# Optimization experiments

Measured on AMD Instinct MI355X. Metric: run time of the kernel, lower is better.

The kernel has to match this reference:

```python
import jax, jax.numpy as jnp
import numpy as np

BETA = 0.25  # commitment_cost


def setup_inputs() -> dict:
    key = jax.random.key(0)
    k1, k2 = jax.random.split(key)
    N, K, D = 32768, 8192, 512
    z = jax.random.normal(k1, (N, D), dtype=jnp.float32)
    # mimic nn.init.uniform_(codebook, -1/K, 1/K)
    codebook = jax.random.uniform(k2, (K, D), dtype=jnp.float32,
                                  minval=-1.0 / K, maxval=1.0 / K)
    return {"z": z, "codebook": codebook}


def reference(z, codebook):
    # squared L2 distances: ||z||^2 + ||c||^2 - 2 z c^T   -> [N, K]
    d = (jnp.sum(z * z, axis=1, keepdims=True)
         + jnp.sum(codebook * codebook, axis=1)
         - 2.0 * (z @ codebook.T))
    indices = jnp.argmin(d, axis=1)            # [N] int
    z_q = codebook[indices]                    # [N, D] gather (grad flows to codebook)
    # commit_loss = beta * mse(z.detach(), z_q)
    commit_loss = BETA * jnp.mean((jax.lax.stop_gradient(z) - z_q) ** 2)
    # straight-through estimator
    z_st = z + jax.lax.stop_gradient(z_q - z)
    return z_st, indices, commit_loss
```

## Files before the change

### kernel.cpp

```cpp
#include <hip/hip_runtime.h>
#include <cfloat>
#include <cstdint>
#include <cstddef>

#define N_ROWS 32768
#define K_CODES 8192
#define DIM 512
#define BETA 0.25

typedef unsigned short u16;
typedef _Float16 half8 __attribute__((ext_vector_type(8)));
typedef float f32x4 __attribute__((ext_vector_type(4)));

#define BM 256
#define BN 256
#define BKH 64
#define NKT (DIM / BKH)
#define OVCAP 512
#define DELTA_A 0.4f

#define GLOAD_LDS16(g, l)                                          \
  __builtin_amdgcn_global_load_lds(                                \
      (const __attribute__((address_space(1))) void*)(g),          \
      (__attribute__((address_space(3))) void*)(l), 16, 0, 0)

__device__ inline u16 f2h(float x) {
  union { _Float16 h; u16 u; } c;
  c.h = (_Float16)x;
  return c.u;
}

__global__ __launch_bounds__(256)
void vq_cvt(const float* __restrict__ src, u16* __restrict__ dst, float scale,
            int n8, int* ovcnt_reset) {
  if (ovcnt_reset != nullptr && blockIdx.x == 0 && threadIdx.x == 0) *ovcnt_reset = 0;
  int i = blockIdx.x * 256 + threadIdx.x;
  if (i >= n8) return;
  float4 a = ((const float4*)src)[(size_t)i * 2];
  float4 b = ((const float4*)src)[(size_t)i * 2 + 1];
  uint4 o;
  o.x = (unsigned)f2h(a.x * scale) | ((unsigned)f2h(a.y * scale) << 16);
  o.y = (unsigned)f2h(a.z * scale) | ((unsigned)f2h(a.w * scale) << 16);
  o.z = (unsigned)f2h(b.x * scale) | ((unsigned)f2h(b.y * scale) << 16);
  o.w = (unsigned)f2h(b.z * scale) | ((unsigned)f2h(b.w * scale) << 16);
  ((uint4*)dst)[i] = o;
}

__global__ __launch_bounds__(256)
void vq_s1(const float* __restrict__ z, float* __restrict__ s1out) {
  int row = blockIdx.x * 256 + threadIdx.x;
  const float* p = z + (size_t)row * DIM;
  float lf[4];
#pragma unroll
  for (int L = 0; L < 4; ++L) {
    const float* q = p + L * 128;
    float r[8];
#pragma unroll
    for (int j = 0; j < 8; ++j) r[j] = __fmul_rn(q[j], q[j]);
    for (int i = 8; i < 128; i += 8) {
#pragma unroll
      for (int j = 0; j < 8; ++j)
        r[j] = __fadd_rn(r[j], __fmul_rn(q[i + j], q[i + j]));
    }
    float s01 = __fadd_rn(r[0], r[1]);
    float s23 = __fadd_rn(r[2], r[3]);
    float s45 = __fadd_rn(r[4], r[5]);
    float s67 = __fadd_rn(r[6], r[7]);
    lf[L] = __fadd_rn(__fadd_rn(s01, s23), __fadd_rn(s45, s67));
  }
  s1out[row] = __fadd_rn(__fadd_rn(lf[0], lf[1]), __fadd_rn(lf[2], lf[3]));
}

__global__ __launch_bounds__(512, 2)
void vq_gemm(const u16* __restrict__ zh, const u16* __restrict__ ch,
             float* __restrict__ tilemax, uint2* __restrict__ ovlist,
             int* __restrict__ ovcnt, int gcap) {
  __shared__ u16 Ah[2][BM * BKH];
  __shared__ u16 Bh[2][BN * BKH];
  __shared__ float rmaxw[4][BM];
  __shared__ uint2 obuf[OVCAP];
  __shared__ int ocnt, gbase;
  const int tid = threadIdx.x;
  const int lane = tid & 63;
  const int wid = tid >> 6;
  const int wm = wid >> 2;
  const int wn = wid & 3;
  const int wrow = wm * 128;
  const int wcol = wn * 64;
  const int col0 = blockIdx.x * BN;
  const int row0 = blockIdx.y * BM;
  if (tid == 0) ocnt = 0;

  f32x4 acc[8][4];
#pragma unroll
  for (int m = 0; m < 8; ++m)
#pragma unroll
    for (int n = 0; n < 4; ++n) acc[m][n] = (f32x4){0.f, 0.f, 0.f, 0.f};

  const int srow = tid >> 3;
  const int sslot = (tid & 7) ^ ((tid >> 3) & 7);
  const u16* pa[4];
  const u16* pb[4];
  unsigned lofs[4];
#pragma unroll
  for (int c = 0; c < 4; ++c) {
    pa[c] = zh + (size_t)(row0 + c * 64 + srow) * DIM + sslot * 8;
    pb[c] = ch + (size_t)(col0 + c * 64 + srow) * DIM + sslot * 8;
    lofs[c] = c * 4096 + tid * 8;
  }

  const int oA0 = (wrow + (lane & 15)) * 128;
  const int oB0 = (wcol + (lane & 15)) * 128;
  int colk[2];
#pragma unroll
  for (int ks = 0; ks < 2; ++ks)
    colk[ks] = (((lane >> 4) + 4 * ks) ^ (lane & 7)) << 4;

#pragma unroll
  for (int c = 0; c < 4; ++c) {
    GLOAD_LDS16(pa[c], (u16*)Ah[0] + lofs[c]);
    GLOAD_LDS16(pb[c], (u16*)Bh[0] + lofs[c]);
    pa[c] += BKH;
    pb[c] += BKH;
  }
  __syncthreads();

  for (int t = 0; t < NKT - 1; ++t) {
    const int cur = t & 1, nxt = cur ^ 1;
#pragma unroll
    for (int c = 0; c < 4; ++c) {
      GLOAD_LDS16(pa[c], (u16*)Ah[nxt] + lofs[c]);
      GLOAD_LDS16(pb[c], (u16*)Bh[nxt] + lofs[c]);
      pa[c] += BKH;
      pb[c] += BKH;
    }
#pragma unroll
    for (int ks = 0; ks < 2; ++ks) {
      half8 af[8], bf[4];
#pragma unroll
      for (int m = 0; m < 8; ++m)
        af[m] = *(const half8*)((const char*)Ah[cur] + oA0 + m * 2048 + colk[ks]);
#pragma unroll
      for (int n = 0; n < 4; ++n)
        bf[n] = *(const half8*)((const char*)Bh[cur] + oB0 + n * 2048 + colk[ks]);
#pragma unroll
      for (int m = 0; m < 8; ++m)
#pragma unroll
        for (int n = 0; n < 4; ++n)
          acc[m][n] = __builtin_amdgcn_mfma_f32_16x16x32_f16(af[m], bf[n],
                                                             acc[m][n], 0, 0, 0);
    }
    __syncthreads();
  }
  {
    const int cur = (NKT - 1) & 1;
#pragma unroll
    for (int ks = 0; ks < 2; ++ks) {
      half8 af[8], bf[4];
#pragma unroll
      for (int m = 0; m < 8; ++m)
        af[m] = *(const half8*)((const char*)Ah[cur] + oA0 + m * 2048 + colk[ks]);
#pragma unroll
      for (int n = 0; n < 4; ++n)
        bf[n] = *(const half8*)((const char*)Bh[cur] + oB0 + n * 2048 + colk[ks]);
#pragma unroll
      for (int m = 0; m < 8; ++m)
#pragma unroll
        for (int n = 0; n < 4; ++n)
          acc[m][n] = __builtin_amdgcn_mfma_f32_16x16x32_f16(af[m], bf[n],
                                                             acc[m][n], 0, 0, 0);
    }
  }

#pragma unroll
  for (int m = 0; m < 8; ++m) {
#pragma unroll
    for (int rg = 0; rg < 4; ++rg) {
      float mx = acc[m][0][rg];
#pragma unroll
      for (int n = 1; n < 4; ++n) mx = fmaxf(mx, acc[m][n][rg]);
#pragma unroll
      for (int s = 1; s <= 8; s <<= 1) mx = fmaxf(mx, __shfl_xor(mx, s, 64));
      int Rloc = wrow + m * 16 + (lane >> 4) * 4 + rg;
      if ((lane & 15) == 0) rmaxw[wn][Rloc] = mx;
    }
  }
  __syncthreads();
#pragma unroll
  for (int m = 0; m < 8; ++m) {
#pragma unroll
    for (int rg = 0; rg < 4; ++rg) {
      int Rloc = wrow + m * 16 + (lane >> 4) * 4 + rg;
      int grow = row0 + Rloc;
      float gm = fmaxf(fmaxf(rmaxw[0][Rloc], rmaxw[1][Rloc]),
                       fmaxf(rmaxw[2][Rloc], rmaxw[3][Rloc]));
      if (wn == 0 && (lane & 15) == 0)
        tilemax[(size_t)blockIdx.x * N_ROWS + grow] = gm;
      float thr = gm - DELTA_A;
#pragma unroll
      for (int n = 0; n < 4; ++n) {
        float v = acc[m][n][rg];
        if (v >= thr) {
          int code = col0 + wcol + n * 16 + (lane & 15);
          uint2 e = make_uint2(((unsigned)grow << 13) | (unsigned)code,
                               __float_as_uint(v));
          int p = atomicAdd(&ocnt, 1);
          if (p < OVCAP) obuf[p] = e;
          else {
            int g = atomicAdd(ovcnt, 1);
            if (g < gcap) ovlist[g] = e;
          }
        }
      }
    }
  }
  __syncthreads();
  int n = ocnt < OVCAP ? ocnt : OVCAP;
  if (tid == 0) gbase = atomicAdd(ovcnt, n);
  __syncthreads();
  for (int i = tid; i < n; i += 512) {
    int g = gbase + i;
    if (g < gcap) ovlist[g] = obuf[i];
  }
}

__global__ __launch_bounds__(256)
void vq_merge(const float* __restrict__ tilemax, float* __restrict__ mthr,
              unsigned long long* __restrict__ win) {
  int row = blockIdx.x * 256 + threadIdx.x;
  float g = -1e30f;
  for (int t = 0; t < K_CODES / BN; ++t)
    g = fmaxf(g, tilemax[(size_t)t * N_ROWS + row]);
  mthr[row] = g - DELTA_A;
  win[row] = ~0ULL;
}

__global__ __launch_bounds__(256)
void vq_init(unsigned long long* __restrict__ win) {
  int row = blockIdx.x * 256 + threadIdx.x;
  win[row] = ~0ULL;
}

__global__ __launch_bounds__(256)
void vq_overflow(const float* __restrict__ z, const float* __restrict__ cb,
                 const float* __restrict__ s1, const float* __restrict__ mthr,
                 const uint2* __restrict__ ovlist, const int* __restrict__ ovcnt,
                 int gcap, unsigned long long* __restrict__ win) {
  int n = *ovcnt;
  if (n > gcap) n = gcap;
  for (int i = blockIdx.x * 256 + threadIdx.x; i < n; i += gridDim.x * 256) {
    uint2 e = ovlist[i];
    int row = e.x >> 13;
    int code = e.x & 8191;
    if (__uint_as_float(e.y) < mthr[row]) continue;
    const float* zp = z + (size_t)row * DIM;
    const float* cp = cb + (size_t)code * DIM;
    float acc = 0.f;
    for (int k = 0; k < DIM; k += 4) {
      float4 zv = *(const float4*)(zp + k);
      float4 cv = *(const float4*)(cp + k);
      acc = fmaf(zv.x, cv.x, acc);
      acc = fmaf(zv.y, cv.y, acc);
      acc = fmaf(zv.z, cv.z, acc);
      acc = fmaf(zv.w, cv.w, acc);
    }
    float dq = __fsub_rn(s1[row], __fmul_rn(2.0f, acc));
    unsigned long long key =
        ((unsigned long long)__float_as_uint(dq) << 32) | (unsigned)code;
    atomicMin(&win[row], key);
  }
}

__global__ __launch_bounds__(256)
void vq_fallback(const float* __restrict__ z, const float* __restrict__ cb,
                 const float* __restrict__ s1, const int* __restrict__ ovcnt,
                 int gcap, int force, unsigned long long* __restrict__ win) {
  if (!force && *ovcnt <= gcap) return;
  __shared__ float zrow[DIM];
  __shared__ unsigned long long red[256];
  for (int row = blockIdx.x; row < N_ROWS; row += gridDim.x) {
    __syncthreads();
    for (int t = threadIdx.x; t < DIM; t += 256) zrow[t] = z[(size_t)row * DIM + t];
    __syncthreads();
    float s1v = s1[row];
    unsigned long long best = ~0ULL;
    for (int j = threadIdx.x; j < K_CODES; j += 256) {
      const float* cp = cb + (size_t)j * DIM;
      float acc = 0.f;
      for (int k = 0; k < DIM; ++k) acc = fmaf(zrow[k], cp[k], acc);
      float dq = __fsub_rn(s1v, __fmul_rn(2.0f, acc));
      unsigned long long key =
          ((unsigned long long)__float_as_uint(dq) << 32) | (unsigned)j;
      if (key < best) best = key;
    }
    red[threadIdx.x] = best;
    __syncthreads();
    for (int s = 128; s > 0; s >>= 1) {
      if (threadIdx.x < s && red[threadIdx.x + s] < red[threadIdx.x])
        red[threadIdx.x] = red[threadIdx.x + s];
      __syncthreads();
    }
    if (threadIdx.x == 0) atomicMin(&win[row], red[0]);
    __syncthreads();
  }
}

__global__ __launch_bounds__(256)
void vq_out(const float* __restrict__ z, const float* __restrict__ cb,
            const unsigned long long* __restrict__ win, float* __restrict__ out,
            double* __restrict__ loss64) {
  int wid = threadIdx.x >> 6, lane = threadIdx.x & 63;
  int row = blockIdx.x * 4 + wid;
  int I1 = (int)(win[row] & 8191ULL);
  const float* zp = z + (size_t)row * DIM + lane * 8;
  const float* cp = cb + (size_t)I1 * DIM + lane * 8;
  float4 z0 = *(const float4*)zp, z1 = *(const float4*)(zp + 4);
  float4 c0 = *(const float4*)cp, c1 = *(const float4*)(cp + 4);
  *(float4*)&out[(size_t)row * DIM + lane * 8] = c0;
  *(float4*)&out[(size_t)row * DIM + lane * 8 + 4] = c1;
  double s = 0.0, d;
  d = (double)z0.x - c0.x; s += d * d;
  d = (double)z0.y - c0.y; s += d * d;
  d = (double)z0.z - c0.z; s += d * d;
  d = (double)z0.w - c0.w; s += d * d;
  d = (double)z1.x - c1.x; s += d * d;
  d = (double)z1.y - c1.y; s += d * d;
  d = (double)z1.z - c1.z; s += d * d;
  d = (double)z1.w - c1.w; s += d * d;
#pragma unroll
  for (int m = 32; m >= 1; m >>= 1) s += __shfl_down(s, m, 64);
  if (lane == 0) {
    loss64[row] = s;
    out[(size_t)N_ROWS * DIM + row] = (float)I1;
  }
}

__global__ __launch_bounds__(1024)
void vq_loss(const double* __restrict__ loss64, float* __restrict__ out) {
  __shared__ double sd[1024];
  double s = 0.0;
  for (int i = threadIdx.x; i < N_ROWS; i += 1024) s += loss64[i];
  sd[threadIdx.x] = s;
  __syncthreads();
  for (int k = 512; k > 0; k >>= 1) {
    if (threadIdx.x < k) sd[threadIdx.x] += sd[threadIdx.x + k];
    __syncthreads();
  }
  if (threadIdx.x == 0)
    out[(size_t)N_ROWS * DIM + N_ROWS] =
        (float)(BETA * sd[0] / ((double)N_ROWS * (double)DIM));
}

extern "C" void kernel_launch(void* const* d_in, const int* in_sizes, int n_in,
                              void* d_out, int out_size, void* d_ws, size_t ws_size,
                              hipStream_t stream) {
  const float* z = (const float*)d_in[0];
  const float* cb = (const float*)d_in[1];
  float* out = (float*)d_out;
  char* ws = (char*)d_ws;

  const size_t OFF_ZH = 0;
  const size_t OFF_CH = 33554432;
  const size_t OFF_S1 = 41943040;
  const size_t OFF_MT = 42074112;
  const size_t OFF_WIN = 42205184;
  const size_t OFF_L64 = 42467328;
  const size_t OFF_TM = 42729472;
  const size_t OFF_OC = 51118080;
  const size_t OFF_OV = 51118096;
  const size_t MIN_FAST = OFF_OV + (size_t)8 * 1024 * 1024;

  if (ws_size >= MIN_FAST) {
    u16* zh = (u16*)(ws + OFF_ZH);
    u16* ch = (u16*)(ws + OFF_CH);
    float* s1f = (float*)(ws + OFF_S1);
    float* mthr = (float*)(ws + OFF_MT);
    unsigned long long* win = (unsigned long long*)(ws + OFF_WIN);
    double* loss64 = (double*)(ws + OFF_L64);
    float* tilemax = (float*)(ws + OFF_TM);
    int* ovcnt = (int*)(ws + OFF_OC);
    uint2* ovlist = (uint2*)(ws + OFF_OV);
    long long gc = (long long)(ws_size - OFF_OV) / 8;
    if (gc > 6 * 1024 * 1024) gc = 6 * 1024 * 1024;
    int gcap = (int)gc;

    vq_cvt<<<N_ROWS * DIM / 8 / 256, 256, 0, stream>>>(z, zh, 1.0f,
                                                       N_ROWS * DIM / 8, ovcnt);
    vq_cvt<<<K_CODES * DIM / 8 / 256, 256, 0, stream>>>(cb, ch, 4096.0f,
                                                        K_CODES * DIM / 8, nullptr);
    vq_s1<<<N_ROWS / 256, 256, 0, stream>>>(z, s1f);
    vq_gemm<<<dim3(K_CODES / BN, N_ROWS / BM), 512, 0, stream>>>(
        zh, ch, tilemax, ovlist, ovcnt, gcap);
    vq_merge<<<N_ROWS / 256, 256, 0, stream>>>(tilemax, mthr, win);
    vq_overflow<<<2048, 256, 0, stream>>>(z, cb, s1f, mthr, ovlist, ovcnt, gcap, win);
    vq_fallback<<<2048, 256, 0, stream>>>(z, cb, s1f, ovcnt, gcap, 0, win);
    vq_out<<<N_ROWS / 4, 256, 0, stream>>>(z, cb, win, out, loss64);
    vq_loss<<<1, 1024, 0, stream>>>(loss64, out);
  } else {
    float* s1f = (float*)(ws + 0);
    unsigned long long* win = (unsigned long long*)(ws + 131072);
    double* loss64 = (double*)(ws + 393216);
    vq_s1<<<N_ROWS / 256, 256, 0, stream>>>(z, s1f);
    vq_init<<<N_ROWS / 256, 256, 0, stream>>>(win);
    vq_fallback<<<2048, 256, 0, stream>>>(z, cb, s1f, nullptr, 0, 1, win);
    vq_out<<<N_ROWS / 4, 256, 0, stream>>>(z, cb, win, out, loss64);
    vq_loss<<<1, 1024, 0, stream>>>(loss64, out);
  }
}
```

Before: 676.5 us.

## Replace double-buffered K loop with 4-slot ring and explicit waitcnt pipelining

The GEMM main loop moves from a two-buffer, 64-wide K step with __syncthreads to a four-slot LDS ring of 32-wide K stages. Loads are issued two stages ahead, and the code waits with explicit vmcnt/lgkmcnt counts and a raw s_barrier instead of full syncthreads. MFMA blocks are wrapped in s_setprio to favour matrix issue. The aim is to keep more global-to-LDS traffic in flight and cut barrier stalls, at the cost of more barriers per K and a new swizzle whose correctness depends on the waitcnt accounting. LDS use stays the same as before.

```diff
diff --git a/kernel.cpp b/kernel.cpp
--- a/kernel.cpp
+++ b/kernel.cpp
@@ -14,8 +14,8 @@
 
 #define BM 256
 #define BN 256
-#define BKH 64
-#define NKT (DIM / BKH)
+#define SKH 32
+#define NPH (DIM / SKH)
 #define OVCAP 512
 #define DELTA_A 0.4f
 
@@ -75,18 +75,15 @@
 void vq_gemm(const u16* __restrict__ zh, const u16* __restrict__ ch,
              float* __restrict__ tilemax, uint2* __restrict__ ovlist,
              int* __restrict__ ovcnt, int gcap) {
-  __shared__ u16 Ah[2][BM * BKH];
-  __shared__ u16 Bh[2][BN * BKH];
+  __shared__ u16 ring[4][16384];
   __shared__ float rmaxw[4][BM];
   __shared__ uint2 obuf[OVCAP];
   __shared__ int ocnt, gbase;
   const int tid = threadIdx.x;
   const int lane = tid & 63;
   const int wid = tid >> 6;
-  const int wm = wid >> 2;
-  const int wn = wid & 3;
-  const int wrow = wm * 128;
-  const int wcol = wn * 64;
+  const int wrow = (wid >> 2) * 128;
+  const int wcol = (wid & 3) * 64;
   const int col0 = blockIdx.x * BN;
   const int row0 = blockIdx.y * BM;
   if (tid == 0) ocnt = 0;
@@ -97,81 +94,64 @@
 #pragma unroll
     for (int n = 0; n < 4; ++n) acc[m][n] = (f32x4){0.f, 0.f, 0.f, 0.f};
 
-  const int srow = tid >> 3;
-  const int sslot = (tid & 7) ^ ((tid >> 3) & 7);
-  const u16* pa[4];
-  const u16* pb[4];
-  unsigned lofs[4];
-#pragma unroll
-  for (int c = 0; c < 4; ++c) {
-    pa[c] = zh + (size_t)(row0 + c * 64 + srow) * DIM + sslot * 8;
-    pb[c] = ch + (size_t)(col0 + c * 64 + srow) * DIM + sslot * 8;
-    lofs[c] = c * 4096 + tid * 8;
-  }
-
-  const int oA0 = (wrow + (lane & 15)) * 128;
-  const int oB0 = (wcol + (lane & 15)) * 128;
-  int colk[2];
-#pragma unroll
-  for (int ks = 0; ks < 2; ++ks)
-    colk[ks] = (((lane >> 4) + 4 * ks) ^ (lane & 7)) << 4;
-
-#pragma unroll
-  for (int c = 0; c < 4; ++c) {
-    GLOAD_LDS16(pa[c], (u16*)Ah[0] + lofs[c]);
-    GLOAD_LDS16(pb[c], (u16*)Bh[0] + lofs[c]);
-    pa[c] += BKH;
-    pb[c] += BKH;
-  }
-  __syncthreads();
-
-  for (int t = 0; t < NKT - 1; ++t) {
-    const int cur = t & 1, nxt = cur ^ 1;
-#pragma unroll
-    for (int c = 0; c < 4; ++c) {
-      GLOAD_LDS16(pa[c], (u16*)Ah[nxt] + lofs[c]);
-      GLOAD_LDS16(pb[c], (u16*)Bh[nxt] + lofs[c]);
-      pa[c] += BKH;
-      pb[c] += BKH;
-    }
-#pragma unroll
-    for (int ks = 0; ks < 2; ++ks) {
-      half8 af[8], bf[4];
-#pragma unroll
-      for (int m = 0; m < 8; ++m)
-        af[m] = *(const half8*)((const char*)Ah[cur] + oA0 + m * 2048 + colk[ks]);
+  const int arow = tid >> 2;
+  const int sslot8 = (((tid & 3) ^ ((tid >> 3) & 3))) * 8;
+  const u16* pa0 = zh + (size_t)(row0 + arow) * DIM + sslot8;
+  const u16* pa1 = pa0 + (size_t)128 * DIM;
+  const u16* pb0 = ch + (size_t)(col0 + arow) * DIM + sslot8;
+  const u16* pb1 = pb0 + (size_t)128 * DIM;
+  const unsigned dof = tid * 8;
+
+#define STAGE(s)                                              \
+  {                                                           \
+    u16* sl_ = ring[(s) & 3];                                 \
+    GLOAD_LDS16(pa0 + (s) * SKH, sl_ + dof);                  \
+    GLOAD_LDS16(pa1 + (s) * SKH, sl_ + 4096 + dof);           \
+    GLOAD_LDS16(pb0 + (s) * SKH, sl_ + 8192 + dof);           \
+    GLOAD_LDS16(pb1 + (s) * SKH, sl_ + 12288 + dof);          \
+  }
+
+  const int xorv = ((lane >> 4) ^ ((lane >> 1) & 3)) << 4;
+  const int aoff = (wrow + (lane & 15)) * 64 + xorv;
+  const int boff = 16384 + (wcol + (lane & 15)) * 64 + xorv;
+
+  STAGE(0);
+  STAGE(1);
+
+#pragma unroll
+  for (int s = 0; s < NPH; ++s) {
+    if (s + 2 < NPH) STAGE(s + 2);
+    if (s < NPH - 2) {
+      asm volatile("s_waitcnt vmcnt(8)" ::: "memory");
+    } else if (s == NPH - 2) {
+      asm volatile("s_waitcnt vmcnt(4)" ::: "memory");
+    } else {
+      asm volatile("s_waitcnt vmcnt(0)" ::: "memory");
+    }
+    __builtin_amdgcn_sched_barrier(0);
+    __builtin_amdgcn_s_barrier();
+    const char* sl = (const char*)ring[s & 3];
+    half8 af[8], bf[4];
+#pragma unroll
+    for (int m = 0; m < 8; ++m)
+      af[m] = *(const half8*)(sl + aoff + m * 1024);
+#pragma unroll
+    for (int n = 0; n < 4; ++n)
+      bf[n] = *(const half8*)(sl + boff + n * 1024);
+    asm volatile("s_waitcnt lgkmcnt(0)" ::: "memory");
+    __builtin_amdgcn_sched_barrier(0);
+    __builtin_amdgcn_s_setprio(1);
+#pragma unroll
+    for (int m = 0; m < 8; ++m)
 #pragma unroll
       for (int n = 0; n < 4; ++n)
-        bf[n] = *(const half8*)((const char*)Bh[cur] + oB0 + n * 2048 + colk[ks]);
-#pragma unroll
-      for (int m = 0; m < 8; ++m)
-#pragma unroll
-        for (int n = 0; n < 4; ++n)
-          acc[m][n] = __builtin_amdgcn_mfma_f32_16x16x32_f16(af[m], bf[n],
-                                                             acc[m][n], 0, 0, 0);
-    }
-    __syncthreads();
-  }
-  {
-    const int cur = (NKT - 1) & 1;
-#pragma unroll
-    for (int ks = 0; ks < 2; ++ks) {
-      half8 af[8], bf[4];
-#pragma unroll
-      for (int m = 0; m < 8; ++m)
-        af[m] = *(const half8*)((const char*)Ah[cur] + oA0 + m * 2048 + colk[ks]);
-#pragma unroll
-      for (int n = 0; n < 4; ++n)
-        bf[n] = *(const half8*)((const char*)Bh[cur] + oB0 + n * 2048 + colk[ks]);
-#pragma unroll
-      for (int m = 0; m < 8; ++m)
-#pragma unroll
-        for (int n = 0; n < 4; ++n)
-          acc[m][n] = __builtin_amdgcn_mfma_f32_16x16x32_f16(af[m], bf[n],
-                                                             acc[m][n], 0, 0, 0);
-    }
-  }
-
+        acc[m][n] = __builtin_amdgcn_mfma_f32_16x16x32_f16(af[m], bf[n],
+                                                           acc[m][n], 0, 0, 0);
+    __builtin_amdgcn_s_setprio(0);
+  }
+#undef STAGE
+
+  const int wn = wid & 3;
 #pragma unroll
   for (int m = 0; m < 8; ++m) {
 #pragma unroll
```

Result: no change. 679.9 us (+0.5%).
